# Kernel tuning notes

Hardware: AMD Instinct MI355X
Metric: run time of the kernel (lower is better)

The kernel has to match this reference:

```python
import jax, jax.numpy as jnp
import numpy as np

B, T, D, H = 4, 2048, 1024, 16
HD = D // H


def setup_inputs() -> dict:
    key = jax.random.key(0)
    k1, k2, k3 = jax.random.split(key, 3)
    x = jax.random.normal(k1, (B, T, D), dtype=jnp.float32)
    # xavier-uniform-like scale for the projections
    s_qkv = float(np.sqrt(6.0 / (D + 3 * D)))
    s_o = float(np.sqrt(6.0 / (D + D)))
    W_qkv = jax.random.uniform(k2, (D, 3 * D), minval=-s_qkv, maxval=s_qkv, dtype=jnp.float32)
    W_o = jax.random.uniform(k3, (D, D), minval=-s_o, maxval=s_o, dtype=jnp.float32)
    b_qkv = jnp.zeros((3 * D,), dtype=jnp.float32)
    b_o = jnp.zeros((D,), dtype=jnp.float32)
    # pad out the last 256 key positions to exercise the padding-mask path
    key_padding_mask = jnp.zeros((B, T), dtype=bool).at[:, -256:].set(True)
    return {"x": x, "W_qkv": W_qkv, "b_qkv": b_qkv, "W_o": W_o, "b_o": b_o,
            "key_padding_mask": key_padding_mask}


def reference(x, W_qkv, b_qkv, W_o, b_o, key_padding_mask):
    Bx, Tx, Dx = x.shape
    # fused QKV projection
    qkv = x @ W_qkv + b_qkv                      # [B,T,3D]
    q, k, v = jnp.split(qkv, 3, axis=-1)
    to_heads = lambda t: t.reshape(Bx, Tx, H, HD).transpose(0, 2, 1, 3)  # [B,H,T,Hd]
    q, k, v = to_heads(q), to_heads(k), to_heads(v)
    scale = 1.0 / np.sqrt(HD).astype(np.float32)
    scores = jnp.einsum('bhqd,bhkd->bhqk', q, k) * scale   # [B,H,T,T]
    causal = jnp.triu(jnp.ones((Tx, Tx), dtype=bool), k=1)  # True above diagonal => masked
    mask = key_padding_mask[:, None, None, :] | causal[None, None, :, :]
    scores = jnp.where(mask, -jnp.inf, scores)
    A = jax.nn.softmax(scores, axis=-1)
    ctx = jnp.einsum('bhqk,bhkd->bhqd', A, v)               # [B,H,T,Hd]
    y = ctx.transpose(0, 2, 1, 3).reshape(Bx, Tx, Dx)
    return y @ W_o + b_o
```

## Files before the change

kernel.cpp:

```cpp
#include <hip/hip_runtime.h>
#include <cstdint>
#include <cstddef>

typedef __bf16 bf16x8 __attribute__((ext_vector_type(8)));
typedef float f32x4 __attribute__((ext_vector_type(4)));
typedef float f32x16 __attribute__((ext_vector_type(16)));
typedef unsigned short u16x4 __attribute__((ext_vector_type(4)));
typedef unsigned int u32x4 __attribute__((ext_vector_type(4)));

__device__ __forceinline__ unsigned short f2bf(float f) {
  union { float f; unsigned u; } v; v.f = f;
  unsigned r = (v.u + 0x7FFF + ((v.u >> 16) & 1)) >> 16;
  return (unsigned short)r;
}

__device__ __forceinline__ unsigned pkbf(float x, float y) {
  unsigned short a = __builtin_bit_cast(unsigned short, (__bf16)x);
  unsigned short b = __builtin_bit_cast(unsigned short, (__bf16)y);
  return (unsigned)a | ((unsigned)b << 16);
}

__device__ __forceinline__ void gl2lds16(const void* g, void* l) {
  __builtin_amdgcn_global_load_lds(
      (const __attribute__((address_space(1))) void*)g,
      (__attribute__((address_space(3))) void*)l,
      16, 0, 0);
}

__global__ __launch_bounds__(256) void cast_f32_bf16(
    const float* __restrict__ in, unsigned short* __restrict__ out, int n) {
  int i = (blockIdx.x * 256 + threadIdx.x) * 4;
  if (i >= n) return;
  float4 v = *(const float4*)(in + i);
  u16x4 o;
  o[0] = f2bf(v.x); o[1] = f2bf(v.y); o[2] = f2bf(v.z); o[3] = f2bf(v.w);
  *(u16x4*)(out + i) = o;
}

__global__ __launch_bounds__(256) void transpose_cast(
    const float* __restrict__ in, unsigned short* __restrict__ out, int R, int C) {
  __shared__ float t[32][33];
  int c0 = blockIdx.x * 32, r0 = blockIdx.y * 32;
  int tx = threadIdx.x, ty = threadIdx.y;
#pragma unroll
  for (int j = 0; j < 4; ++j)
    t[ty + j * 8][tx] = in[(size_t)(r0 + ty + j * 8) * C + c0 + tx];
  __syncthreads();
#pragma unroll
  for (int j = 0; j < 4; ++j)
    out[(size_t)(c0 + ty + j * 8) * R + r0 + tx] = f2bf(t[tx][ty + j * 8]);
}

__global__ __launch_bounds__(256) void prep_pad(
    const int* __restrict__ mask, float* __restrict__ padd, int* __restrict__ kmax, int n) {
  int i = blockIdx.x * 256 + threadIdx.x;
  if (i >= n) return;
  int mv = mask[i];
  padd[i] = mv ? -1e30f : 0.0f;
  int key = mv ? 0 : ((i & 2047) + 1);
#pragma unroll
  for (int off = 32; off; off >>= 1) key = max(key, __shfl_xor(key, off, 64));
  if ((threadIdx.x & 63) == 0) atomicMax(&kmax[i >> 11], key);
}

template <int EPI>
__global__ __launch_bounds__(256) void gemm_bt(
    const unsigned short* __restrict__ A, const unsigned short* __restrict__ Bm,
    const float* __restrict__ bias, float* __restrict__ outF,
    unsigned short* __restrict__ Qb, unsigned short* __restrict__ Kb,
    unsigned short* __restrict__ Vt, int M, int N, int K) {
  __shared__ unsigned short As[128 * 32];
  __shared__ unsigned short Bs[128 * 32];
  const int tid = threadIdx.x;
  const int bm = blockIdx.x * 128;
  const int bn = blockIdx.y * 128;
  const int wave = tid >> 6, lane = tid & 63;
  const int wm = (wave >> 1) * 64, wn = (wave & 1) * 64;
  const int lr = lane & 15, lq = lane >> 4;

  f32x4 acc[4][4] = {};

  const int c0 = tid, c1 = tid + 256;
  const int rA0 = c0 >> 2, colA0 = (c0 & 3) * 8;
  const int rA1 = c1 >> 2, colA1 = (c1 & 3) * 8;

  for (int k0 = 0; k0 < K; k0 += 32) {
    __syncthreads();
    gl2lds16(A + (size_t)(bm + rA0) * K + k0 + colA0, As + c0 * 8);
    gl2lds16(A + (size_t)(bm + rA1) * K + k0 + colA1, As + c1 * 8);
    gl2lds16(Bm + (size_t)(bn + rA0) * K + k0 + colA0, Bs + c0 * 8);
    gl2lds16(Bm + (size_t)(bn + rA1) * K + k0 + colA1, Bs + c1 * 8);
    __syncthreads();
    bf16x8 af[4], bfr[4];
#pragma unroll
    for (int mi = 0; mi < 4; ++mi)
      af[mi] = *(const bf16x8*)(As + (wm + mi * 16 + lr) * 32 + lq * 8);
#pragma unroll
    for (int nj = 0; nj < 4; ++nj)
      bfr[nj] = *(const bf16x8*)(Bs + (wn + nj * 16 + lr) * 32 + lq * 8);
#pragma unroll
    for (int mi = 0; mi < 4; ++mi)
#pragma unroll
      for (int nj = 0; nj < 4; ++nj)
        acc[mi][nj] = __builtin_amdgcn_mfma_f32_16x16x32_bf16(af[mi], bfr[nj], acc[mi][nj], 0, 0, 0);
  }

#pragma unroll
  for (int mi = 0; mi < 4; ++mi) {
#pragma unroll
    for (int nj = 0; nj < 4; ++nj) {
#pragma unroll
      for (int r = 0; r < 4; ++r) {
        int m = bm + wm + mi * 16 + lq * 4 + r;
        int n = bn + wn + nj * 16 + lr;
        float v = acc[mi][nj][r] + bias[n];
        if (EPI == 0) {
          int b = m >> 11, t = m & 2047;
          int part = n >> 10, d = n & 1023;
          int h = d >> 6, hd = d & 63;
          size_t qk = ((size_t)(b * 16 + h) * 2048 + t) * 64 + hd;
          if (part == 0)      Qb[qk] = f2bf(v * 0.18033688011112042f);
          else if (part == 1) Kb[qk] = f2bf(v);
          else                Vt[((size_t)(b * 16 + h) * 64 + hd) * 2048 + t] = f2bf(v);
        } else {
          outF[(size_t)m * N + n] = v;
        }
      }
    }
  }
}


__global__ __launch_bounds__(256, 2) void flash_attn(
    const unsigned short* __restrict__ Qb, const unsigned short* __restrict__ Kb,
    const unsigned short* __restrict__ Vt, const int* __restrict__ kmax,
    unsigned short* __restrict__ ctx) {
  __shared__ unsigned short lds[16384];

  const int bid = blockIdx.x;
  const int halfg = bid >> 8;
  const int rb = bid & 255;
  const int bh = rb & 63;
  const int jj = rb >> 6;
  const int j = halfg ? (7 - jj) : jj;
  const int blockQ = j << 8;
  const int b = bh >> 4, h = bh & 15;
  const int tid = threadIdx.x;
  const int wave = tid >> 6, lane = tid & 63;
  const int l31 = lane & 31, hi = lane >> 5;
  const int qw = blockQ + wave * 64;

  const unsigned short* Qh = Qb + (size_t)bh * 2048 * 64;
  const unsigned short* Kh = Kb + (size_t)bh * 2048 * 64;
  const unsigned short* Vh = Vt + (size_t)bh * 64 * 2048;
  unsigned short* ctxBase = ctx + (size_t)b * 2048 * 1024 + h * 64;

  const int kmaxRaw = kmax[b];
  const int kcapC = (kmaxRaw + 63) >> 6;
  const int lastB = min((blockQ + 255) >> 6, kcapC - 1);
  const int diagI = qw >> 6;

  bf16x8 qf[2][4];
#pragma unroll
  for (int qt = 0; qt < 2; ++qt)
#pragma unroll
    for (int ds = 0; ds < 4; ++ds)
      qf[qt][ds] = *(const bf16x8*)(Qh + (size_t)(qw + qt * 32 + l31) * 64 + ds * 16 + hi * 8);

  f32x16 O[2][2] = {};
  float mR[2] = {-1e30f, -1e30f}, lR[2] = {0.f, 0.f};

  const int trow = tid >> 3, tslot = tid & 7;

  auto stage = [&](int bufI, int kcS) {
#pragma unroll
    for (int rnd = 0; rnd < 2; ++rnd) {
      int row = rnd * 32 + trow;
      int sl = tslot ^ (row & 7);
      gl2lds16(Kh + (size_t)(kcS + row) * 64 + sl * 8,
               lds + bufI * 8192 + rnd * 2048 + tid * 8);
      gl2lds16(Vh + (size_t)row * 2048 + kcS + sl * 8,
               lds + bufI * 8192 + 4096 + rnd * 2048 + tid * 8);
    }
  };

  stage(0, 0);
  int cur = 0;
  for (int i = 0; i <= lastB; ++i) {
    __syncthreads();
    if (i < lastB) stage(cur ^ 1, (i + 1) << 6);
    if (i <= diagI) {
      const int kc = i << 6;
      const unsigned short* Ksb = lds + cur * 8192;
      const unsigned short* Vsb = Ksb + 4096;

      f32x16 S[2][2] = {};
      __builtin_amdgcn_s_setprio(1);
#pragma unroll
      for (int kt = 0; kt < 2; ++kt) {
        const int row = kt * 32 + l31;
        const int rx = row & 7;
#pragma unroll
        for (int ds = 0; ds < 4; ++ds) {
          bf16x8 kfr = *(const bf16x8*)(Ksb + row * 64 + (((ds * 2 + hi) ^ rx) << 3));
          S[0][kt] = __builtin_amdgcn_mfma_f32_32x32x16_bf16(kfr, qf[0][ds], S[0][kt], 0, 0, 0);
          S[1][kt] = __builtin_amdgcn_mfma_f32_32x32x16_bf16(kfr, qf[1][ds], S[1][kt], 0, 0, 0);
        }
      }
      __builtin_amdgcn_s_setprio(0);

      const bool isDiag = (i == diagI);
      if (isDiag || (kc + 64 > kmaxRaw)) {
#pragma unroll
        for (int qt = 0; qt < 2; ++qt) {
          const int q = qw + qt * 32 + l31;
#pragma unroll
          for (int kt = 0; kt < 2; ++kt)
#pragma unroll
            for (int rr = 0; rr < 16; ++rr) {
              int key = kc + kt * 32 + (rr & 3) + ((rr >> 2) << 3) + (hi << 2);
              if ((isDiag && key > q) || key >= kmaxRaw) S[qt][kt][rr] = -1e30f;
            }
        }
      }

      bf16x8 pf[2][2][2];
#pragma unroll
      for (int qt = 0; qt < 2; ++qt) {
        float v[16];
#pragma unroll
        for (int rr = 0; rr < 16; ++rr) v[rr] = fmaxf(S[qt][0][rr], S[qt][1][rr]);
#pragma unroll
        for (int st = 8; st; st >>= 1)
#pragma unroll
          for (int rr = 0; rr < st; ++rr) v[rr] = fmaxf(v[rr], v[rr + st]);
        float mx = fmaxf(v[0], __shfl_xor(v[0], 32, 64));
        float mnew = fmaxf(mR[qt], mx);
        float a = __builtin_amdgcn_exp2f(mR[qt] - mnew);
        mR[qt] = mnew;
#pragma unroll
        for (int kt = 0; kt < 2; ++kt)
#pragma unroll
          for (int rr = 0; rr < 16; ++rr)
            S[qt][kt][rr] = __builtin_amdgcn_exp2f(S[qt][kt][rr] - mnew);
        float sacc[16];
#pragma unroll
        for (int rr = 0; rr < 16; ++rr) sacc[rr] = S[qt][0][rr] + S[qt][1][rr];
#pragma unroll
        for (int st = 8; st; st >>= 1)
#pragma unroll
          for (int rr = 0; rr < st; ++rr) sacc[rr] += sacc[rr + st];
        float sum = sacc[0] + __shfl_xor(sacc[0], 32, 64);
        lR[qt] = lR[qt] * a + sum;
#pragma unroll
        for (int mt = 0; mt < 2; ++mt)
#pragma unroll
          for (int rr = 0; rr < 16; ++rr) O[qt][mt][rr] *= a;
#pragma unroll
        for (int kt = 0; kt < 2; ++kt) {
          unsigned a0 = pkbf(S[qt][kt][0], S[qt][kt][1]);
          unsigned a1 = pkbf(S[qt][kt][2], S[qt][kt][3]);
          unsigned b0 = pkbf(S[qt][kt][4], S[qt][kt][5]);
          unsigned b1 = pkbf(S[qt][kt][6], S[qt][kt][7]);
          unsigned c0 = pkbf(S[qt][kt][8], S[qt][kt][9]);
          unsigned c1 = pkbf(S[qt][kt][10], S[qt][kt][11]);
          unsigned d0 = pkbf(S[qt][kt][12], S[qt][kt][13]);
          unsigned d1 = pkbf(S[qt][kt][14], S[qt][kt][15]);
          unsigned s0 = __shfl_xor(hi ? a0 : b0, 32, 64);
          unsigned s1 = __shfl_xor(hi ? a1 : b1, 32, 64);
          unsigned s2 = __shfl_xor(hi ? c0 : d0, 32, 64);
          unsigned s3 = __shfl_xor(hi ? c1 : d1, 32, 64);
          u32x4 f0, f1;
          f0[0] = hi ? s0 : a0; f0[1] = hi ? s1 : a1;
          f0[2] = hi ? b0 : s0; f0[3] = hi ? b1 : s1;
          f1[0] = hi ? s2 : c0; f1[1] = hi ? s3 : c1;
          f1[2] = hi ? d0 : s2; f1[3] = hi ? d1 : s3;
          pf[qt][kt][0] = __builtin_bit_cast(bf16x8, f0);
          pf[qt][kt][1] = __builtin_bit_cast(bf16x8, f1);
        }
      }

      __builtin_amdgcn_s_setprio(1);
      const int vx = l31 & 7;
#pragma unroll
      for (int kt = 0; kt < 2; ++kt)
#pragma unroll
        for (int ks = 0; ks < 2; ++ks) {
          const int slot = kt * 4 + ks * 2 + hi;
          bf16x8 v0 = *(const bf16x8*)(Vsb + l31 * 64 + ((slot ^ vx) << 3));
          bf16x8 v1 = *(const bf16x8*)(Vsb + (32 + l31) * 64 + ((slot ^ vx) << 3));
          O[0][0] = __builtin_amdgcn_mfma_f32_32x32x16_bf16(v0, pf[0][kt][ks], O[0][0], 0, 0, 0);
          O[0][1] = __builtin_amdgcn_mfma_f32_32x32x16_bf16(v1, pf[0][kt][ks], O[0][1], 0, 0, 0);
          O[1][0] = __builtin_amdgcn_mfma_f32_32x32x16_bf16(v0, pf[1][kt][ks], O[1][0], 0, 0, 0);
          O[1][1] = __builtin_amdgcn_mfma_f32_32x32x16_bf16(v1, pf[1][kt][ks], O[1][1], 0, 0, 0);
        }
      __builtin_amdgcn_s_setprio(0);
    }
    cur ^= 1;
  }

#pragma unroll
  for (int qt = 0; qt < 2; ++qt) {
    float linv = 1.0f / lR[qt];
    const int q = qw + qt * 32 + l31;
    unsigned short* cp = ctxBase + (size_t)q * 1024;
#pragma unroll
    for (int mt = 0; mt < 2; ++mt)
#pragma unroll
      for (int g = 0; g < 4; ++g) {
        u16x4 o4;
#pragma unroll
        for (int rr = 0; rr < 4; ++rr) o4[rr] = f2bf(O[qt][mt][4 * g + rr] * linv);
        *(u16x4*)(cp + mt * 32 + 8 * g + 4 * hi) = o4;
      }
  }
}

extern "C" void kernel_launch(void* const* d_in, const int* in_sizes, int n_in,
                              void* d_out, int out_size, void* d_ws, size_t ws_size,
                              hipStream_t stream) {
  const float* x    = (const float*)d_in[0];
  const float* Wqkv = (const float*)d_in[1];
  const float* bqkv = (const float*)d_in[2];
  const float* Wo   = (const float*)d_in[3];
  const float* bo   = (const float*)d_in[4];
  const int*   mask = (const int*)d_in[5];
  float* out = (float*)d_out;

  unsigned short* ws = (unsigned short*)d_ws;
  const size_t SZ_X = (size_t)8192 * 1024;
  unsigned short* xb    = ws;
  unsigned short* WqkvT = xb + SZ_X;
  unsigned short* WoT   = WqkvT + (size_t)3072 * 1024;
  unsigned short* Qb    = WoT + (size_t)1024 * 1024;
  unsigned short* Kb    = Qb + SZ_X;
  unsigned short* Vt    = Kb + SZ_X;
  float*          padd  = (float*)(Vt + SZ_X);
  int*            kmax  = (int*)(padd + 8192);
  unsigned short* ctx   = xb;

  hipMemsetAsync(kmax, 0, 4 * sizeof(int), stream);
  cast_f32_bf16<<<8192, 256, 0, stream>>>(x, xb, (int)SZ_X);
  transpose_cast<<<dim3(96, 32), dim3(32, 8), 0, stream>>>(Wqkv, WqkvT, 1024, 3072);
  transpose_cast<<<dim3(32, 32), dim3(32, 8), 0, stream>>>(Wo, WoT, 1024, 1024);
  prep_pad<<<32, 256, 0, stream>>>(mask, padd, kmax, 8192);
  gemm_bt<0><<<dim3(64, 24), 256, 0, stream>>>(xb, WqkvT, bqkv, nullptr, Qb, Kb, Vt,
                                               8192, 3072, 1024);
  flash_attn<<<512, 256, 0, stream>>>(Qb, Kb, Vt, kmax, ctx);
  gemm_bt<1><<<dim3(64, 8), 256, 0, stream>>>(ctx, WoT, bo, out, nullptr, nullptr, nullptr,
                                              8192, 1024, 1024);
}
```

Baseline: 296.2 us.

## Double-buffer GEMM LDS tiles and halve attention query tile per block

The GEMM kernel now double-buffers its A/B LDS tiles, issuing the next k-slice's global-to-LDS loads before computing on the current one and dropping one barrier per iteration. The flash attention kernel drops from 256 to 128 query rows per block (32 per wave). This doubles the grid to 1024 blocks and raises launch bounds to 4 blocks per CU, aiming for better occupancy and causal load balance. The cost is that each K/V tile loaded into LDS now feeds half as many queries, so K/V traffic roughly doubles. The GEMM change also doubles its LDS footprint.

```diff
diff --git a/kernel.cpp b/kernel.cpp
--- a/kernel.cpp
+++ b/kernel.cpp
@@ -69,8 +69,8 @@
     const float* __restrict__ bias, float* __restrict__ outF,
     unsigned short* __restrict__ Qb, unsigned short* __restrict__ Kb,
     unsigned short* __restrict__ Vt, int M, int N, int K) {
-  __shared__ unsigned short As[128 * 32];
-  __shared__ unsigned short Bs[128 * 32];
+  __shared__ unsigned short As[2 * 128 * 32];
+  __shared__ unsigned short Bs[2 * 128 * 32];
   const int tid = threadIdx.x;
   const int bm = blockIdx.x * 128;
   const int bn = blockIdx.y * 128;
@@ -84,25 +84,33 @@
   const int rA0 = c0 >> 2, colA0 = (c0 & 3) * 8;
   const int rA1 = c1 >> 2, colA1 = (c1 & 3) * 8;
 
+  auto stage = [&](int buf, int k0) {
+    gl2lds16(A + (size_t)(bm + rA0) * K + k0 + colA0, As + buf * 4096 + c0 * 8);
+    gl2lds16(A + (size_t)(bm + rA1) * K + k0 + colA1, As + buf * 4096 + c1 * 8);
+    gl2lds16(Bm + (size_t)(bn + rA0) * K + k0 + colA0, Bs + buf * 4096 + c0 * 8);
+    gl2lds16(Bm + (size_t)(bn + rA1) * K + k0 + colA1, Bs + buf * 4096 + c1 * 8);
+  };
+
+  stage(0, 0);
+  int cur = 0;
   for (int k0 = 0; k0 < K; k0 += 32) {
     __syncthreads();
-    gl2lds16(A + (size_t)(bm + rA0) * K + k0 + colA0, As + c0 * 8);
-    gl2lds16(A + (size_t)(bm + rA1) * K + k0 + colA1, As + c1 * 8);
-    gl2lds16(Bm + (size_t)(bn + rA0) * K + k0 + colA0, Bs + c0 * 8);
-    gl2lds16(Bm + (size_t)(bn + rA1) * K + k0 + colA1, Bs + c1 * 8);
-    __syncthreads();
+    if (k0 + 32 < K) stage(cur ^ 1, k0 + 32);
+    const unsigned short* Asb = As + cur * 4096;
+    const unsigned short* Bsb = Bs + cur * 4096;
     bf16x8 af[4], bfr[4];
 #pragma unroll
     for (int mi = 0; mi < 4; ++mi)
-      af[mi] = *(const bf16x8*)(As + (wm + mi * 16 + lr) * 32 + lq * 8);
+      af[mi] = *(const bf16x8*)(Asb + (wm + mi * 16 + lr) * 32 + lq * 8);
 #pragma unroll
     for (int nj = 0; nj < 4; ++nj)
-      bfr[nj] = *(const bf16x8*)(Bs + (wn + nj * 16 + lr) * 32 + lq * 8);
+      bfr[nj] = *(const bf16x8*)(Bsb + (wn + nj * 16 + lr) * 32 + lq * 8);
 #pragma unroll
     for (int mi = 0; mi < 4; ++mi)
 #pragma unroll
       for (int nj = 0; nj < 4; ++nj)
         acc[mi][nj] = __builtin_amdgcn_mfma_f32_16x16x32_bf16(af[mi], bfr[nj], acc[mi][nj], 0, 0, 0);
+    cur ^= 1;
   }
 
 #pragma unroll
@@ -130,25 +138,24 @@
   }
 }
 
-
-__global__ __launch_bounds__(256, 2) void flash_attn(
+__global__ __launch_bounds__(256, 4) void flash_attn(
     const unsigned short* __restrict__ Qb, const unsigned short* __restrict__ Kb,
     const unsigned short* __restrict__ Vt, const int* __restrict__ kmax,
     unsigned short* __restrict__ ctx) {
   __shared__ unsigned short lds[16384];
 
   const int bid = blockIdx.x;
-  const int halfg = bid >> 8;
-  const int rb = bid & 255;
+  const int halfg = bid >> 9;
+  const int rb = bid & 511;
   const int bh = rb & 63;
-  const int jj = rb >> 6;
-  const int j = halfg ? (7 - jj) : jj;
-  const int blockQ = j << 8;
+  const int j0 = rb >> 6;
+  const int j = halfg ? (15 - j0) : j0;
+  const int blockQ = j << 7;
   const int b = bh >> 4, h = bh & 15;
   const int tid = threadIdx.x;
   const int wave = tid >> 6, lane = tid & 63;
   const int l31 = lane & 31, hi = lane >> 5;
-  const int qw = blockQ + wave * 64;
+  const int qw = blockQ + wave * 32;
 
   const unsigned short* Qh = Qb + (size_t)bh * 2048 * 64;
   const unsigned short* Kh = Kb + (size_t)bh * 2048 * 64;
@@ -157,18 +164,16 @@
 
   const int kmaxRaw = kmax[b];
   const int kcapC = (kmaxRaw + 63) >> 6;
-  const int lastB = min((blockQ + 255) >> 6, kcapC - 1);
+  const int lastB = min((blockQ + 127) >> 6, kcapC - 1);
   const int diagI = qw >> 6;
 
-  bf16x8 qf[2][4];
-#pragma unroll
-  for (int qt = 0; qt < 2; ++qt)
-#pragma unroll
-    for (int ds = 0; ds < 4; ++ds)
-      qf[qt][ds] = *(const bf16x8*)(Qh + (size_t)(qw + qt * 32 + l31) * 64 + ds * 16 + hi * 8);
-
-  f32x16 O[2][2] = {};
-  float mR[2] = {-1e30f, -1e30f}, lR[2] = {0.f, 0.f};
+  bf16x8 qf[4];
+#pragma unroll
+  for (int ds = 0; ds < 4; ++ds)
+    qf[ds] = *(const bf16x8*)(Qh + (size_t)(qw + l31) * 64 + ds * 16 + hi * 8);
+
+  f32x16 O[2] = {};
+  float mR = -1e30f, lR = 0.f;
 
   const int trow = tid >> 3, tslot = tid & 7;
 
@@ -194,7 +199,7 @@
       const unsigned short* Ksb = lds + cur * 8192;
       const unsigned short* Vsb = Ksb + 4096;
 
-      f32x16 S[2][2] = {};
+      f32x16 S[2] = {};
       __builtin_amdgcn_s_setprio(1);
 #pragma unroll
       for (int kt = 0; kt < 2; ++kt) {
@@ -203,81 +208,76 @@
 #pragma unroll
         for (int ds = 0; ds < 4; ++ds) {
           bf16x8 kfr = *(const bf16x8*)(Ksb + row * 64 + (((ds * 2 + hi) ^ rx) << 3));
-          S[0][kt] = __builtin_amdgcn_mfma_f32_32x32x16_bf16(kfr, qf[0][ds], S[0][kt], 0, 0, 0);
-          S[1][kt] = __builtin_amdgcn_mfma_f32_32x32x16_bf16(kfr, qf[1][ds], S[1][kt], 0, 0, 0);
+          S[kt] = __builtin_amdgcn_mfma_f32_32x32x16_bf16(kfr, qf[ds], S[kt], 0, 0, 0);
         }
       }
       __builtin_amdgcn_s_setprio(0);
 
       const bool isDiag = (i == diagI);
       if (isDiag || (kc + 64 > kmaxRaw)) {
-#pragma unroll
-        for (int qt = 0; qt < 2; ++qt) {
-          const int q = qw + qt * 32 + l31;
-#pragma unroll
-          for (int kt = 0; kt < 2; ++kt)
-#pragma unroll
-            for (int rr = 0; rr < 16; ++rr) {
-              int key = kc + kt * 32 + (rr & 3) + ((rr >> 2) << 3) + (hi << 2);
-              if ((isDiag && key > q) || key >= kmaxRaw) S[qt][kt][rr] = -1e30f;
-            }
-        }
-      }
-
-      bf16x8 pf[2][2][2];
-#pragma unroll
-      for (int qt = 0; qt < 2; ++qt) {
+        const int q = qw + l31;
+#pragma unroll
+        for (int kt = 0; kt < 2; ++kt)
+#pragma unroll
+          for (int rr = 0; rr < 16; ++rr) {
+            int key = kc + kt * 32 + (rr & 3) + ((rr >> 2) << 3) + (hi << 2);
+            if ((isDiag && key > q) || key >= kmaxRaw) S[kt][rr] = -1e30f;
+          }
+      }
+
+      {
         float v[16];
 #pragma unroll
-        for (int rr = 0; rr < 16; ++rr) v[rr] = fmaxf(S[qt][0][rr], S[qt][1][rr]);
+        for (int rr = 0; rr < 16; ++rr) v[rr] = fmaxf(S[0][rr], S[1][rr]);
 #pragma unroll
         for (int st = 8; st; st >>= 1)
 #pragma unroll
           for (int rr = 0; rr < st; ++rr) v[rr] = fmaxf(v[rr], v[rr + st]);
         float mx = fmaxf(v[0], __shfl_xor(v[0], 32, 64));
-        float mnew = fmaxf(mR[qt], mx);
-        float a = __builtin_amdgcn_exp2f(mR[qt] - mnew);
-        mR[qt] = mnew;
+        float mnew = fmaxf(mR, mx);
+        float a = __builtin_amdgcn_exp2f(mR - mnew);
+        mR = mnew;
 #pragma unroll
         for (int kt = 0; kt < 2; ++kt)
 #pragma unroll
           for (int rr = 0; rr < 16; ++rr)
-            S[qt][kt][rr] = __builtin_amdgcn_exp2f(S[qt][kt][rr] - mnew);
+            S[kt][rr] = __builtin_amdgcn_exp2f(S[kt][rr] - mnew);
         float sacc[16];
 #pragma unroll
-        for (int rr = 0; rr < 16; ++rr) sacc[rr] = S[qt][0][rr] + S[qt][1][rr];
+        for (int rr = 0; rr < 16; ++rr) sacc[rr] = S[0][rr] + S[1][rr];
 #pragma unroll
         for (int st = 8; st; st >>= 1)
 #pragma unroll
           for (int rr = 0; rr < st; ++rr) sacc[rr] += sacc[rr + st];
         float sum = sacc[0] + __shfl_xor(sacc[0], 32, 64);
-        lR[qt] = lR[qt] * a + sum;
+        lR = lR * a + sum;
 #pragma unroll
         for (int mt = 0; mt < 2; ++mt)
 #pragma unroll
-          for (int rr = 0; rr < 16; ++rr) O[qt][mt][rr] *= a;
-#pragma unroll
-        for (int kt = 0; kt < 2; ++kt) {
-          unsigned a0 = pkbf(S[qt][kt][0], S[qt][kt][1]);
-          unsigned a1 = pkbf(S[qt][kt][2], S[qt][kt][3]);
-          unsigned b0 = pkbf(S[qt][kt][4], S[qt][kt][5]);
-          unsigned b1 = pkbf(S[qt][kt][6], S[qt][kt][7]);
-          unsigned c0 = pkbf(S[qt][kt][8], S[qt][kt][9]);
-          unsigned c1 = pkbf(S[qt][kt][10], S[qt][kt][11]);
-          unsigned d0 = pkbf(S[qt][kt][12], S[qt][kt][13]);
-          unsigned d1 = pkbf(S[qt][kt][14], S[qt][kt][15]);
-          unsigned s0 = __shfl_xor(hi ? a0 : b0, 32, 64);
-          unsigned s1 = __shfl_xor(hi ? a1 : b1, 32, 64);
-          unsigned s2 = __shfl_xor(hi ? c0 : d0, 32, 64);
-          unsigned s3 = __shfl_xor(hi ? c1 : d1, 32, 64);
-          u32x4 f0, f1;
-          f0[0] = hi ? s0 : a0; f0[1] = hi ? s1 : a1;
-          f0[2] = hi ? b0 : s0; f0[3] = hi ? b1 : s1;
-          f1[0] = hi ? s2 : c0; f1[1] = hi ? s3 : c1;
-          f1[2] = hi ? d0 : s2; f1[3] = hi ? d1 : s3;
-          pf[qt][kt][0] = __builtin_bit_cast(bf16x8, f0);
-          pf[qt][kt][1] = __builtin_bit_cast(bf16x8, f1);
-        }
+          for (int rr = 0; rr < 16; ++rr) O[mt][rr] *= a;
+      }
+      bf16x8 pf[2][2];
+#pragma unroll
+      for (int kt = 0; kt < 2; ++kt) {
+        unsigned a0 = pkbf(S[kt][0], S[kt][1]);
+        unsigned a1 = pkbf(S[kt][2], S[kt][3]);
+        unsigned b0 = pkbf(S[kt][4], S[kt][5]);
+        unsigned b1 = pkbf(S[kt][6], S[kt][7]);
+        unsigned c0 = pkbf(S[kt][8], S[kt][9]);
+        unsigned c1 = pkbf(S[kt][10], S[kt][11]);
+        unsigned d0 = pkbf(S[kt][12], S[kt][13]);
+        unsigned d1 = pkbf(S[kt][14], S[kt][15]);
+        unsigned s0 = __shfl_xor(hi ? a0 : b0, 32, 64);
+        unsigned s1 = __shfl_xor(hi ? a1 : b1, 32, 64);
+        unsigned s2 = __shfl_xor(hi ? c0 : d0, 32, 64);
+        unsigned s3 = __shfl_xor(hi ? c1 : d1, 32, 64);
+        u32x4 f0, f1;
+        f0[0] = hi ? s0 : a0; f0[1] = hi ? s1 : a1;
+        f0[2] = hi ? b0 : s0; f0[3] = hi ? b1 : s1;
+        f1[0] = hi ? s2 : c0; f1[1] = hi ? s3 : c1;
+        f1[2] = hi ? d0 : s2; f1[3] = hi ? d1 : s3;
+        pf[kt][0] = __builtin_bit_cast(bf16x8, f0);
+        pf[kt][1] = __builtin_bit_cast(bf16x8, f1);
       }
 
       __builtin_amdgcn_s_setprio(1);
@@ -289,20 +289,17 @@
           const int slot = kt * 4 + ks * 2 + hi;
           bf16x8 v0 = *(const bf16x8*)(Vsb + l31 * 64 + ((slot ^ vx) << 3));
           bf16x8 v1 = *(const bf16x8*)(Vsb + (32 + l31) * 64 + ((slot ^ vx) << 3));
-          O[0][0] = __builtin_amdgcn_mfma_f32_32x32x16_bf16(v0, pf[0][kt][ks], O[0][0], 0, 0, 0);
-          O[0][1] = __builtin_amdgcn_mfma_f32_32x32x16_bf16(v1, pf[0][kt][ks], O[0][1], 0, 0, 0);
-          O[1][0] = __builtin_amdgcn_mfma_f32_32x32x16_bf16(v0, pf[1][kt][ks], O[1][0], 0, 0, 0);
-          O[1][1] = __builtin_amdgcn_mfma_f32_32x32x16_bf16(v1, pf[1][kt][ks], O[1][1], 0, 0, 0);
+          O[0] = __builtin_amdgcn_mfma_f32_32x32x16_bf16(v0, pf[kt][ks], O[0], 0, 0, 0);
+          O[1] = __builtin_amdgcn_mfma_f32_32x32x16_bf16(v1, pf[kt][ks], O[1], 0, 0, 0);
         }
       __builtin_amdgcn_s_setprio(0);
     }
     cur ^= 1;
   }
 
-#pragma unroll
-  for (int qt = 0; qt < 2; ++qt) {
-    float linv = 1.0f / lR[qt];
-    const int q = qw + qt * 32 + l31;
+  {
+    float linv = 1.0f / lR;
+    const int q = qw + l31;
     unsigned short* cp = ctxBase + (size_t)q * 1024;
 #pragma unroll
     for (int mt = 0; mt < 2; ++mt)
@@ -310,7 +307,7 @@
       for (int g = 0; g < 4; ++g) {
         u16x4 o4;
 #pragma unroll
-        for (int rr = 0; rr < 4; ++rr) o4[rr] = f2bf(O[qt][mt][4 * g + rr] * linv);
+        for (int rr = 0; rr < 4; ++rr) o4[rr] = f2bf(O[mt][4 * g + rr] * linv);
         *(u16x4*)(cp + mt * 32 + 8 * g + 4 * hi) = o4;
       }
   }
@@ -346,7 +343,7 @@
   prep_pad<<<32, 256, 0, stream>>>(mask, padd, kmax, 8192);
   gemm_bt<0><<<dim3(64, 24), 256, 0, stream>>>(xb, WqkvT, bqkv, nullptr, Qb, Kb, Vt,
                                                8192, 3072, 1024);
-  flash_attn<<<512, 256, 0, stream>>>(Qb, Kb, Vt, kmax, ctx);
+  flash_attn<<<1024, 256, 0, stream>>>(Qb, Kb, Vt, kmax, ctx);
   gemm_bt<1><<<dim3(64, 8), 256, 0, stream>>>(ctx, WoT, bo, out, nullptr, nullptr, nullptr,
                                               8192, 1024, 1024);
 }
```

New measurement: 273.7 us. -7.6%, faster.
